# Optimization experiments

Hardware: AMD Instinct MI355X
Metric: run time of the kernel (lower is better)

The kernel has to match this reference:

```python
import jax, jax.numpy as jnp
import numpy as np
from jax import lax

# dims: T timesteps, CIN=6 DoG channels, HxW image; F conv filters, K kernel
T, CIN, H, W_IN = 15, 6, 512, 512
F, K, PAD = 64, 5, 2
THRESH = 15.0
K_WTA, RADIUS = 5, 2  # self.k1, self.r1


def setup_inputs() -> dict:
    key = jax.random.key(0)
    k1, k2 = jax.random.split(key)
    # cumulative binary spike wave: once a unit spikes it stays 1 (SpykeTorch convention)
    ev = (jax.random.uniform(k1, (T, CIN, H, W_IN)) < 0.02).astype(jnp.float32)
    x = jnp.clip(jnp.cumsum(ev, axis=0), 0.0, 1.0)
    w = 0.8 + 0.05 * jax.random.normal(k2, (F, CIN, K, K), dtype=jnp.float32)
    return {"x": x, "w": w}


def _pool_pad(x, pad):
    # sf.pooling(x, 2, 2): max-pool 2x2 stride 2; sf.pad: zero pad
    x = lax.reduce_window(x, -jnp.inf, lax.max, (1, 1, 2, 2), (1, 1, 2, 2), 'VALID')
    return jnp.pad(x, ((0, 0), (0, 0), (pad, pad), (pad, pad)))


def _fire(pot, thr):
    # sf.fire(pot, thr, True): zero sub-threshold potentials, spikes = sign
    tp = jnp.where(pot < thr, 0.0, pot)
    return jnp.sign(tp), tp


def _pointwise_inhibition(pot):
    # keep, per spatial site, only the feature with the earliest (then strongest) spike
    T_ = pot.shape[0]
    max_vals = jnp.max(pot, axis=1, keepdims=True)      # [T,1,H,W]
    max_idx = jnp.argmax(pot, axis=1, keepdims=True)    # [T,1,H,W]
    clamp = jnp.sign(max_vals)                          # 1 where any feature active
    earliest = jnp.clip(T_ - jnp.sum(clamp, axis=0, keepdims=True), 0, T_ - 1).astype(jnp.int32)  # [1,1,H,W]
    winners = jnp.take_along_axis(max_idx, earliest, axis=0)  # [1,1,H,W] winning feature
    has_spike = clamp[-1:]                              # [1,1,H,W] any spike by last step
    ch = jnp.arange(pot.shape[1]).reshape(1, -1, 1, 1)
    coef = jnp.where(ch == winners, has_spike, 0.0)     # scatter of winner coeff
    return pot * coef


def _get_k_winners(pot, spikes, k, radius):
    # NMS-like radius-based k-winners-take-all over [F,H,W]
    T_ = pot.shape[0]
    earliest = jnp.clip(T_ - jnp.sum(spikes, axis=0, keepdims=True), 0, T_ - 1).astype(jnp.int32)
    values = jnp.take_along_axis(pot, earliest, axis=0)  # potential at earliest spike
    trunc = spikes * values
    v = jnp.max(trunc) * T_  # large bias favoring earlier spikes
    total = jnp.sum(trunc + spikes * v, axis=0)          # [F,H,W]
    Fc, Hh, Ww = total.shape
    feat = jnp.arange(Fc).reshape(-1, 1, 1)
    row = jnp.arange(Hh).reshape(1, -1, 1)
    col = jnp.arange(Ww).reshape(1, 1, -1)
    winners = []
    for _ in range(k):  # small fixed k (5), fine to unroll
        idx = jnp.argmax(total)
        val = jnp.reshape(total, (-1,))[idx]
        f, r, c = jnp.unravel_index(idx, total.shape)
        active = val != 0
        win = jnp.where(active, jnp.stack([f, r, c]).astype(jnp.int32),
                        jnp.full((3,), -1, jnp.int32))
        winners.append(win)
        suppress = (feat == f) | ((jnp.abs(row - r) <= radius) & (jnp.abs(col - c) <= radius))
        total = jnp.where(active & suppress, 0.0, total)
    return jnp.stack(winners)  # [k,3] with -1 rows when fewer winners exist


def reference(x, w):
    inp = _pool_pad(x, PAD)  # [T,6,260,260]
    pot = lax.conv_general_dilated(inp, w, (1, 1), 'VALID',
                                   dimension_numbers=('NCHW', 'OIHW', 'NCHW'))  # [T,F,256,256]
    spk, pot = _fire(pot, THRESH)
    pot = _pointwise_inhibition(pot)
    spk = jnp.sign(pot)
    winners = _get_k_winners(pot, spk, K_WTA, RADIUS)
    return spk, winners
```

## Files before the change

kernel.cpp:

```cpp
#include <hip/hip_runtime.h>
#include <hip/hip_bf16.h>

#define T_ 15
#define CIN_ 6
#define F_ 64
#define HW_ 256
#define PW_ 260
#define THRESH_ 15.0f
#define TAU_NEVER 15


__global__ __launch_bounds__(256) void pool_tau(const float* __restrict__ x,
                                                unsigned char* __restrict__ tau,
                                                unsigned long long* __restrict__ slots,
                                                unsigned int* __restrict__ gmaxp) {
    int idx = blockIdx.x * 256 + threadIdx.x;
    if (idx < 5) slots[idx] = 0ULL;
    if (idx == 5) *gmaxp = 0u;
    if (idx >= CIN_ * PW_ * PW_) return;
    int xx = idx % PW_;
    int rest = idx / PW_;
    int yy = rest % PW_;
    int c = rest / PW_;
    unsigned char tv = TAU_NEVER;
    if (xx >= 2 && xx < 258 && yy >= 2 && yy < 258) {
        int i = yy - 2, j = xx - 2;
        const float* b0 = x + ((size_t)c * 512 + 2 * i) * 512 + 2 * j;
        const size_t tstride = (size_t)CIN_ * 512 * 512;
        {
            const float* b = b0 + 14 * tstride;
            float2 a = *(const float2*)b;
            float2 d = *(const float2*)(b + 512);
            if (a.x > 0.f || a.y > 0.f || d.x > 0.f || d.y > 0.f) {
                int lo = 0, hi = 14;
                while (lo < hi) {
                    int mid = (lo + hi) >> 1;
                    const float* bm = b0 + (size_t)mid * tstride;
                    float2 am = *(const float2*)bm;
                    float2 dm = *(const float2*)(bm + 512);
                    bool on = (am.x > 0.f || am.y > 0.f || dm.x > 0.f || dm.y > 0.f);
                    if (on) hi = mid; else lo = mid + 1;
                }
                tv = (unsigned char)lo;
            }
        }
    }
    tau[idx] = tv;
}

__global__ __launch_bounds__(256, 3) void phaseA(const unsigned char* __restrict__ tau,
                                                 const float* __restrict__ w,
                                                 int* __restrict__ rec_wch,
                                                 float* __restrict__ rec_val,
                                                 int* __restrict__ rec_e,
                                                 unsigned int* __restrict__ gmaxp) {
    __shared__ float wl2[150 * 64];
    __shared__ unsigned char tw[CIN_ * 144];
    __shared__ float wmax[4];

    const int tid = threadIdx.x;
    const int lane = tid & 63;
    const int g = tid >> 6;
    const int gx = (g & 1) * 4;
    const int gy = (g >> 1) * 4;
    const int px0 = blockIdx.x * 8;
    const int py0 = blockIdx.y * 8;

    for (int idx = tid; idx < 9600; idx += 256) {
        int k = idx >> 6, f = idx & 63;
        wl2[idx] = w[f * 150 + k];
    }
    for (int idx = tid; idx < CIN_ * 144; idx += 256) {
        int c = idx / 144;
        int rem = idx - c * 144;
        int r = rem / 12;
        int xx = rem - r * 12;
        tw[idx] = tau[(c * PW_ + (py0 + r)) * PW_ + (px0 + xx)];
    }
    __syncthreads();

    unsigned int done = 0;
    int myw = -1, mye = T_;
    float myv = 0.0f;
    float wavemax = 0.0f;

    for (int t = 0; t < T_; ++t) {
        float acc[16];
#pragma unroll
        for (int i = 0; i < 16; ++i) acc[i] = 0.0f;

        for (int c = 0; c < CIN_; ++c) {
            float win[8][8];
            const unsigned char* tb = &tw[c * 144 + gy * 12 + gx];
#pragma unroll
            for (int r = 0; r < 8; ++r) {
                unsigned int lo = *(const unsigned int*)(tb + r * 12);
                unsigned int hi = *(const unsigned int*)(tb + r * 12 + 4);
#pragma unroll
                for (int b = 0; b < 4; ++b) {
                    win[r][b]     = (((lo >> (8 * b)) & 0xFF) <= (unsigned)t) ? 1.0f : 0.0f;
                    win[r][4 + b] = (((hi >> (8 * b)) & 0xFF) <= (unsigned)t) ? 1.0f : 0.0f;
                }
            }
#pragma unroll
            for (int ki = 0; ki < 5; ++ki)
#pragma unroll
                for (int kj = 0; kj < 5; ++kj) {
                    float wv = wl2[((c * 25 + ki * 5 + kj) << 6) + lane];
#pragma unroll
                    for (int py = 0; py < 4; ++py)
#pragma unroll
                        for (int px = 0; px < 4; ++px)
                            acc[py * 4 + px] += win[py + ki][px + kj] * wv;
                }
        }

#pragma unroll
        for (int i = 0; i < 16; ++i) {
            if (done & (1u << i)) continue;
            float v = acc[i];
            v = (v < THRESH_) ? 0.0f : v;
            if (__any(v > 0.0f)) {
                unsigned long long key =
                    ((unsigned long long)__float_as_uint(v) << 6) | (unsigned)(63 - lane);
#pragma unroll
                for (int m = 1; m < 64; m <<= 1) {
                    unsigned long long o = __shfl_xor(key, m, 64);
                    if (o > key) key = o;
                }
                float mv = __uint_as_float((unsigned int)(key >> 6));
                int wf = 63 - (int)(key & 63ULL);
                done |= (1u << i);
                if (lane == i) { myw = wf; myv = mv; mye = t; }
                wavemax = fmaxf(wavemax, mv);
            }
        }
        if (done == 0xFFFFu) break;
    }

    if (lane < 16) {
        int py = lane >> 2, px = lane & 3;
        int p = (py0 + gy + py) * HW_ + (px0 + gx + px);
        rec_wch[p] = myw;
        rec_val[p] = myv;
        rec_e[p] = mye;
    }
    if (lane == 0) wmax[g] = wavemax;
    __syncthreads();
    if (tid == 0) {
        float m = fmaxf(fmaxf(wmax[0], wmax[1]), fmaxf(wmax[2], wmax[3]));
        if (m > 0.0f) atomicMax(gmaxp, __float_as_uint(m));
    }
}

__global__ __launch_bounds__(256) void render(const int* __restrict__ rec_wch,
                                              const int* __restrict__ rec_e,
                                              float* __restrict__ out) {
    const int tid = threadIdx.x;
    const int t = blockIdx.y;
    const int px = blockIdx.x * 1024 + tid * 4;

    int4 wch4 = *(const int4*)(rec_wch + px);
    int4 e4   = *(const int4*)(rec_e + px);
    int s0 = (wch4.x >= 0 && t >= e4.x) ? wch4.x : -1;
    int s1 = (wch4.y >= 0 && t >= e4.y) ? wch4.y : -1;
    int s2 = (wch4.z >= 0 && t >= e4.z) ? wch4.z : -1;
    int s3 = (wch4.w >= 0 && t >= e4.w) ? wch4.w : -1;

    float* base = out + (((size_t)t * F_) << 16) + px;
#pragma unroll
    for (int f = 0; f < F_; ++f) {
        float4 v;
        v.x = (f == s0) ? 1.0f : 0.0f;
        v.y = (f == s1) ? 1.0f : 0.0f;
        v.z = (f == s2) ? 1.0f : 0.0f;
        v.w = (f == s3) ? 1.0f : 0.0f;
        *(float4*)(base + ((size_t)f << 16)) = v;
    }
}

__global__ __launch_bounds__(256) void compute_total(const int* __restrict__ rec_wch,
                                                     const float* __restrict__ rec_val,
                                                     const int* __restrict__ rec_e,
                                                     const unsigned int* __restrict__ gmaxp,
                                                     float* __restrict__ total) {
    int i = blockIdx.x * 256 + threadIdx.x;
    int wch = rec_wch[i];
    float g = __uint_as_float(*gmaxp);
    float v15 = 15.0f * g;
    float tot = 0.0f;
    if (wch >= 0) {
        int e = rec_e[i];
        float base = rec_val[i] + v15;
        for (int t = e; t < T_; ++t) tot += base;
    }
    total[i] = tot;
}

__global__ __launch_bounds__(256) void max_round(const float* __restrict__ total,
                                                 const int* __restrict__ rec_wch,
                                                 unsigned long long* __restrict__ slots,
                                                 int round) {
    __shared__ unsigned long long sred[256];
    int i = blockIdx.x * 256 + threadIdx.x;
    float v = total[i];
    unsigned long long key = 0ULL;
    if (v > 0.0f) {
        int fch = rec_wch[i];
        int r = i >> 8, c = i & 255;
        bool sup = false;
        for (int j = 0; j < round; ++j) {
            unsigned long long s = slots[j];
            if (s == 0ULL) continue;
            int fl = 0x7fffffff - (int)(unsigned int)(s & 0xffffffffu);
            int fj = fl >> 16, rj = (fl >> 8) & 255, cj = fl & 255;
            int dr = r - rj; if (dr < 0) dr = -dr;
            int dc = c - cj; if (dc < 0) dc = -dc;
            if (fch == fj || (dr <= 2 && dc <= 2)) sup = true;
        }
        if (!sup) {
            int fl = (fch << 16) | i;
            unsigned int comp = 0x7fffffffu - (unsigned int)fl;
            key = ((unsigned long long)__float_as_uint(v) << 32) | comp;
        }
    }
    sred[threadIdx.x] = key;
    __syncthreads();
    for (int s = 128; s > 0; s >>= 1) {
        if (threadIdx.x < s) {
            if (sred[threadIdx.x + s] > sred[threadIdx.x]) sred[threadIdx.x] = sred[threadIdx.x + s];
        }
        __syncthreads();
    }
    if (threadIdx.x == 0 && sred[0] != 0ULL)
        atomicMax(&slots[round], sred[0]);
}

__global__ void writer(const unsigned long long* __restrict__ slots,
                       float* __restrict__ out) {
    int r = threadIdx.x;
    if (r < 5) {
        unsigned long long s = slots[r];
        float* wout = out + (size_t)T_ * F_ * HW_ * HW_ + r * 3;
        if (s != 0ULL) {
            int fl = 0x7fffffff - (int)(unsigned int)(s & 0xffffffffu);
            wout[0] = (float)(fl >> 16);
            wout[1] = (float)((fl >> 8) & 255);
            wout[2] = (float)(fl & 255);
        } else {
            wout[0] = -1.0f; wout[1] = -1.0f; wout[2] = -1.0f;
        }
    }
}

extern "C" void kernel_launch(void* const* d_in, const int* in_sizes, int n_in,
                              void* d_out, int out_size, void* d_ws, size_t ws_size,
                              hipStream_t stream) {
    const float* x = (const float*)d_in[0];
    const float* w = (const float*)d_in[1];
    float* out = (float*)d_out;

    char* wsc = (char*)d_ws;
    unsigned char* tau = (unsigned char*)wsc;
    size_t off = (size_t)CIN_ * PW_ * PW_;
    int* rec_wch = (int*)(wsc + off);        off += 65536 * sizeof(int);
    float* rec_val = (float*)(wsc + off);    off += 65536 * sizeof(float);
    int* rec_e = (int*)(wsc + off);          off += 65536 * sizeof(int);
    float* total = (float*)(wsc + off);      off += 65536 * sizeof(float);
    unsigned long long* slots = (unsigned long long*)(wsc + off);  off += 5 * sizeof(unsigned long long);
    unsigned int* gmaxp = (unsigned int*)(wsc + off);

    pool_tau<<<(CIN_ * PW_ * PW_ + 255) / 256, 256, 0, stream>>>(x, tau, slots, gmaxp);
    phaseA<<<dim3(32, 32), 256, 0, stream>>>(tau, w, rec_wch, rec_val, rec_e, gmaxp);
    render<<<dim3(64, 15), 256, 0, stream>>>(rec_wch, rec_e, out);
    compute_total<<<256, 256, 0, stream>>>(rec_wch, rec_val, rec_e, gmaxp, total);
    for (int r = 0; r < 5; ++r)
        max_round<<<256, 256, 0, stream>>>(total, rec_wch, slots, r);
    writer<<<1, 64, 0, stream>>>(slots, out);
}
```

Baseline: 471.3 us.

## Fuse k-winner selection into one single-block kernel and use nontemporal stores

Replaces the total computation, five per-round max-reduction launches and the writer kernel with one 1024-thread block that keeps totals in registers and runs all five suppression rounds with shared-memory reductions. This removes several launches and global round-trips for slots and totals. The render kernel switches its one-hot output writes to nontemporal stores to avoid polluting cache. The risk is that a single block on one compute unit serialises the selection work, and the 64-entry per-thread arrays may spill.

```diff
diff --git a/kernel.cpp b/kernel.cpp
--- a/kernel.cpp
+++ b/kernel.cpp
@@ -9,14 +9,14 @@
 #define THRESH_ 15.0f
 #define TAU_NEVER 15
 
+typedef float v4f __attribute__((ext_vector_type(4)));
+
 
 __global__ __launch_bounds__(256) void pool_tau(const float* __restrict__ x,
                                                 unsigned char* __restrict__ tau,
-                                                unsigned long long* __restrict__ slots,
                                                 unsigned int* __restrict__ gmaxp) {
     int idx = blockIdx.x * 256 + threadIdx.x;
-    if (idx < 5) slots[idx] = 0ULL;
-    if (idx == 5) *gmaxp = 0u;
+    if (idx == 0) *gmaxp = 0u;
     if (idx >= CIN_ * PW_ * PW_) return;
     int xx = idx % PW_;
     int rest = idx / PW_;
@@ -27,22 +27,20 @@
         int i = yy - 2, j = xx - 2;
         const float* b0 = x + ((size_t)c * 512 + 2 * i) * 512 + 2 * j;
         const size_t tstride = (size_t)CIN_ * 512 * 512;
-        {
-            const float* b = b0 + 14 * tstride;
-            float2 a = *(const float2*)b;
-            float2 d = *(const float2*)(b + 512);
-            if (a.x > 0.f || a.y > 0.f || d.x > 0.f || d.y > 0.f) {
-                int lo = 0, hi = 14;
-                while (lo < hi) {
-                    int mid = (lo + hi) >> 1;
-                    const float* bm = b0 + (size_t)mid * tstride;
-                    float2 am = *(const float2*)bm;
-                    float2 dm = *(const float2*)(bm + 512);
-                    bool on = (am.x > 0.f || am.y > 0.f || dm.x > 0.f || dm.y > 0.f);
-                    if (on) hi = mid; else lo = mid + 1;
-                }
-                tv = (unsigned char)lo;
-            }
+        const float* b = b0 + 14 * tstride;
+        float2 a = *(const float2*)b;
+        float2 d = *(const float2*)(b + 512);
+        if (a.x > 0.f || a.y > 0.f || d.x > 0.f || d.y > 0.f) {
+            int lo = 0, hi = 14;
+            while (lo < hi) {
+                int mid = (lo + hi) >> 1;
+                const float* bm = b0 + (size_t)mid * tstride;
+                float2 am = *(const float2*)bm;
+                float2 dm = *(const float2*)(bm + 512);
+                bool on = (am.x > 0.f || am.y > 0.f || dm.x > 0.f || dm.y > 0.f);
+                if (on) hi = mid; else lo = mid + 1;
+            }
+            tv = (unsigned char)lo;
         }
     }
     tau[idx] = tv;
@@ -170,86 +168,88 @@
     float* base = out + (((size_t)t * F_) << 16) + px;
 #pragma unroll
     for (int f = 0; f < F_; ++f) {
-        float4 v;
+        v4f v;
         v.x = (f == s0) ? 1.0f : 0.0f;
         v.y = (f == s1) ? 1.0f : 0.0f;
         v.z = (f == s2) ? 1.0f : 0.0f;
         v.w = (f == s3) ? 1.0f : 0.0f;
-        *(float4*)(base + ((size_t)f << 16)) = v;
-    }
-}
-
-__global__ __launch_bounds__(256) void compute_total(const int* __restrict__ rec_wch,
-                                                     const float* __restrict__ rec_val,
-                                                     const int* __restrict__ rec_e,
-                                                     const unsigned int* __restrict__ gmaxp,
-                                                     float* __restrict__ total) {
-    int i = blockIdx.x * 256 + threadIdx.x;
-    int wch = rec_wch[i];
+        __builtin_nontemporal_store(v, (v4f*)(base + ((size_t)f << 16)));
+    }
+}
+
+__global__ __launch_bounds__(1024) void select_winners(const int* __restrict__ rec_wch,
+                                                       const float* __restrict__ rec_val,
+                                                       const int* __restrict__ rec_e,
+                                                       const unsigned int* __restrict__ gmaxp,
+                                                       float* __restrict__ out) {
+    __shared__ unsigned long long sred[1024];
+    __shared__ int wfj[5], wrj[5], wcj[5], wact[5];
+
+    const int tid = threadIdx.x;
     float g = __uint_as_float(*gmaxp);
     float v15 = 15.0f * g;
-    float tot = 0.0f;
-    if (wch >= 0) {
-        int e = rec_e[i];
-        float base = rec_val[i] + v15;
-        for (int t = e; t < T_; ++t) tot += base;
-    }
-    total[i] = tot;
-}
-
-__global__ __launch_bounds__(256) void max_round(const float* __restrict__ total,
-                                                 const int* __restrict__ rec_wch,
-                                                 unsigned long long* __restrict__ slots,
-                                                 int round) {
-    __shared__ unsigned long long sred[256];
-    int i = blockIdx.x * 256 + threadIdx.x;
-    float v = total[i];
-    unsigned long long key = 0ULL;
-    if (v > 0.0f) {
-        int fch = rec_wch[i];
-        int r = i >> 8, c = i & 255;
-        bool sup = false;
-        for (int j = 0; j < round; ++j) {
-            unsigned long long s = slots[j];
-            if (s == 0ULL) continue;
-            int fl = 0x7fffffff - (int)(unsigned int)(s & 0xffffffffu);
-            int fj = fl >> 16, rj = (fl >> 8) & 255, cj = fl & 255;
-            int dr = r - rj; if (dr < 0) dr = -dr;
-            int dc = c - cj; if (dc < 0) dc = -dc;
-            if (fch == fj || (dr <= 2 && dc <= 2)) sup = true;
-        }
-        if (!sup) {
-            int fl = (fch << 16) | i;
-            unsigned int comp = 0x7fffffffu - (unsigned int)fl;
-            key = ((unsigned long long)__float_as_uint(v) << 32) | comp;
-        }
-    }
-    sred[threadIdx.x] = key;
-    __syncthreads();
-    for (int s = 128; s > 0; s >>= 1) {
-        if (threadIdx.x < s) {
-            if (sred[threadIdx.x + s] > sred[threadIdx.x]) sred[threadIdx.x] = sred[threadIdx.x + s];
-        }
+
+    float tot[64];
+    signed char fc[64];
+#pragma unroll 4
+    for (int k = 0; k < 64; ++k) {
+        int i = k * 1024 + tid;
+        int wch = rec_wch[i];
+        float tt = 0.0f;
+        if (wch >= 0) {
+            int e = rec_e[i];
+            float base = rec_val[i] + v15;
+            for (int t = e; t < T_; ++t) tt += base;
+        }
+        tot[k] = tt;
+        fc[k] = (signed char)wch;
+    }
+
+    for (int round = 0; round < 5; ++round) {
+        unsigned long long key = 0ULL;
+        for (int k = 0; k < 64; ++k) {
+            float v = tot[k];
+            if (v <= 0.0f) continue;
+            int i = k * 1024 + tid;
+            int fch = fc[k];
+            int r = i >> 8, c = i & 255;
+            bool sup = false;
+            for (int j = 0; j < round; ++j) {
+                if (!wact[j]) continue;
+                int dr = r - wrj[j]; if (dr < 0) dr = -dr;
+                int dc = c - wcj[j]; if (dc < 0) dc = -dc;
+                if (fch == wfj[j] || (dr <= 2 && dc <= 2)) sup = true;
+            }
+            if (!sup) {
+                int fl = (fch << 16) | i;
+                unsigned int comp = 0x7fffffffu - (unsigned int)fl;
+                unsigned long long kk =
+                    ((unsigned long long)__float_as_uint(v) << 32) | comp;
+                if (kk > key) key = kk;
+            }
+        }
+        sred[tid] = key;
         __syncthreads();
-    }
-    if (threadIdx.x == 0 && sred[0] != 0ULL)
-        atomicMax(&slots[round], sred[0]);
-}
-
-__global__ void writer(const unsigned long long* __restrict__ slots,
-                       float* __restrict__ out) {
-    int r = threadIdx.x;
-    if (r < 5) {
-        unsigned long long s = slots[r];
-        float* wout = out + (size_t)T_ * F_ * HW_ * HW_ + r * 3;
-        if (s != 0ULL) {
-            int fl = 0x7fffffff - (int)(unsigned int)(s & 0xffffffffu);
-            wout[0] = (float)(fl >> 16);
-            wout[1] = (float)((fl >> 8) & 255);
-            wout[2] = (float)(fl & 255);
-        } else {
-            wout[0] = -1.0f; wout[1] = -1.0f; wout[2] = -1.0f;
-        }
+        for (int s = 512; s > 0; s >>= 1) {
+            if (tid < s) {
+                if (sred[tid + s] > sred[tid]) sred[tid] = sred[tid + s];
+            }
+            __syncthreads();
+        }
+        if (tid == 0) {
+            unsigned long long sk = sred[0];
+            float* wout = out + (size_t)T_ * F_ * HW_ * HW_ + round * 3;
+            if (sk != 0ULL) {
+                int fl = 0x7fffffff - (int)(unsigned int)(sk & 0xffffffffu);
+                int f = fl >> 16, r = (fl >> 8) & 255, c = fl & 255;
+                wfj[round] = f; wrj[round] = r; wcj[round] = c; wact[round] = 1;
+                wout[0] = (float)f; wout[1] = (float)r; wout[2] = (float)c;
+            } else {
+                wact[round] = 0;
+                wout[0] = -1.0f; wout[1] = -1.0f; wout[2] = -1.0f;
+            }
+        }
+        __syncthreads();
     }
 }
 
@@ -266,15 +266,10 @@
     int* rec_wch = (int*)(wsc + off);        off += 65536 * sizeof(int);
     float* rec_val = (float*)(wsc + off);    off += 65536 * sizeof(float);
     int* rec_e = (int*)(wsc + off);          off += 65536 * sizeof(int);
-    float* total = (float*)(wsc + off);      off += 65536 * sizeof(float);
-    unsigned long long* slots = (unsigned long long*)(wsc + off);  off += 5 * sizeof(unsigned long long);
     unsigned int* gmaxp = (unsigned int*)(wsc + off);
 
-    pool_tau<<<(CIN_ * PW_ * PW_ + 255) / 256, 256, 0, stream>>>(x, tau, slots, gmaxp);
+    pool_tau<<<(CIN_ * PW_ * PW_ + 255) / 256, 256, 0, stream>>>(x, tau, gmaxp);
     phaseA<<<dim3(32, 32), 256, 0, stream>>>(tau, w, rec_wch, rec_val, rec_e, gmaxp);
     render<<<dim3(64, 15), 256, 0, stream>>>(rec_wch, rec_e, out);
-    compute_total<<<256, 256, 0, stream>>>(rec_wch, rec_val, rec_e, gmaxp, total);
-    for (int r = 0; r < 5; ++r)
-        max_round<<<256, 256, 0, stream>>>(total, rec_wch, slots, r);
-    writer<<<1, 64, 0, stream>>>(slots, out);
-}
+    select_winners<<<1, 1024, 0, stream>>>(rec_wch, rec_val, rec_e, gmaxp, out);
+}
```

Result: slower. 764.2 us (+62.2%).

## Precompute packed winner keys and use wavefront-shuffle reductions in k-WTA rounds

Applied to the files above, without the earlier changes.

Spike rendering now uses nontemporal vector stores for the large 15x64x256x256 output. The total-potential pass is replaced by a kernel that packs value and location into 64-bit keys, four pixels per thread. Each max round then reads only those keys and decodes earlier winners once per thread instead of per pixel. The shared-memory tree reduction is replaced with wavefront shuffles and one atomicMax per wavefront. The key buffer is larger than the old total buffer, but the small per-round kernels launch fewer blocks and do less synchronisation.

```diff
diff --git a/kernel.cpp b/kernel.cpp
--- a/kernel.cpp
+++ b/kernel.cpp
@@ -8,6 +8,8 @@
 #define PW_ 260
 #define THRESH_ 15.0f
 #define TAU_NEVER 15
+
+typedef float v4f __attribute__((ext_vector_type(4)));
 
 
 __global__ __launch_bounds__(256) void pool_tau(const float* __restrict__ x,
@@ -27,22 +29,20 @@
         int i = yy - 2, j = xx - 2;
         const float* b0 = x + ((size_t)c * 512 + 2 * i) * 512 + 2 * j;
         const size_t tstride = (size_t)CIN_ * 512 * 512;
-        {
-            const float* b = b0 + 14 * tstride;
-            float2 a = *(const float2*)b;
-            float2 d = *(const float2*)(b + 512);
-            if (a.x > 0.f || a.y > 0.f || d.x > 0.f || d.y > 0.f) {
-                int lo = 0, hi = 14;
-                while (lo < hi) {
-                    int mid = (lo + hi) >> 1;
-                    const float* bm = b0 + (size_t)mid * tstride;
-                    float2 am = *(const float2*)bm;
-                    float2 dm = *(const float2*)(bm + 512);
-                    bool on = (am.x > 0.f || am.y > 0.f || dm.x > 0.f || dm.y > 0.f);
-                    if (on) hi = mid; else lo = mid + 1;
-                }
-                tv = (unsigned char)lo;
-            }
+        const float* b = b0 + 14 * tstride;
+        float2 a = *(const float2*)b;
+        float2 d = *(const float2*)(b + 512);
+        if (a.x > 0.f || a.y > 0.f || d.x > 0.f || d.y > 0.f) {
+            int lo = 0, hi = 14;
+            while (lo < hi) {
+                int mid = (lo + hi) >> 1;
+                const float* bm = b0 + (size_t)mid * tstride;
+                float2 am = *(const float2*)bm;
+                float2 dm = *(const float2*)(bm + 512);
+                bool on = (am.x > 0.f || am.y > 0.f || dm.x > 0.f || dm.y > 0.f);
+                if (on) hi = mid; else lo = mid + 1;
+            }
+            tv = (unsigned char)lo;
         }
     }
     tau[idx] = tv;
@@ -170,70 +170,83 @@
     float* base = out + (((size_t)t * F_) << 16) + px;
 #pragma unroll
     for (int f = 0; f < F_; ++f) {
-        float4 v;
+        v4f v;
         v.x = (f == s0) ? 1.0f : 0.0f;
         v.y = (f == s1) ? 1.0f : 0.0f;
         v.z = (f == s2) ? 1.0f : 0.0f;
         v.w = (f == s3) ? 1.0f : 0.0f;
-        *(float4*)(base + ((size_t)f << 16)) = v;
-    }
-}
-
-__global__ __launch_bounds__(256) void compute_total(const int* __restrict__ rec_wch,
-                                                     const float* __restrict__ rec_val,
-                                                     const int* __restrict__ rec_e,
-                                                     const unsigned int* __restrict__ gmaxp,
-                                                     float* __restrict__ total) {
-    int i = blockIdx.x * 256 + threadIdx.x;
-    int wch = rec_wch[i];
+        __builtin_nontemporal_store(v, (v4f*)(base + ((size_t)f << 16)));
+    }
+}
+
+__global__ __launch_bounds__(256) void build_keys(const int* __restrict__ rec_wch,
+                                                  const float* __restrict__ rec_val,
+                                                  const int* __restrict__ rec_e,
+                                                  const unsigned int* __restrict__ gmaxp,
+                                                  unsigned long long* __restrict__ keys) {
+    int i0 = (blockIdx.x * 256 + threadIdx.x) * 4;
     float g = __uint_as_float(*gmaxp);
     float v15 = 15.0f * g;
-    float tot = 0.0f;
-    if (wch >= 0) {
-        int e = rec_e[i];
-        float base = rec_val[i] + v15;
-        for (int t = e; t < T_; ++t) tot += base;
-    }
-    total[i] = tot;
-}
-
-__global__ __launch_bounds__(256) void max_round(const float* __restrict__ total,
-                                                 const int* __restrict__ rec_wch,
+    int4 wch4 = *(const int4*)(rec_wch + i0);
+    float4 val4 = *(const float4*)(rec_val + i0);
+    int4 e4 = *(const int4*)(rec_e + i0);
+#pragma unroll
+    for (int q = 0; q < 4; ++q) {
+        int wch = (q == 0) ? wch4.x : (q == 1) ? wch4.y : (q == 2) ? wch4.z : wch4.w;
+        float val = (q == 0) ? val4.x : (q == 1) ? val4.y : (q == 2) ? val4.z : val4.w;
+        int e = (q == 0) ? e4.x : (q == 1) ? e4.y : (q == 2) ? e4.z : e4.w;
+        unsigned long long key = 0ULL;
+        if (wch >= 0) {
+            float base = val + v15;
+            float tot = 0.0f;
+            for (int t = e; t < T_; ++t) tot += base;
+            if (tot > 0.0f) {
+                int fl = (wch << 16) | (i0 + q);
+                key = ((unsigned long long)__float_as_uint(tot) << 32)
+                    | (0x7fffffffu - (unsigned int)fl);
+            }
+        }
+        keys[i0 + q] = key;
+    }
+}
+
+__global__ __launch_bounds__(256) void max_round(const unsigned long long* __restrict__ keys,
                                                  unsigned long long* __restrict__ slots,
                                                  int round) {
-    __shared__ unsigned long long sred[256];
-    int i = blockIdx.x * 256 + threadIdx.x;
-    float v = total[i];
-    unsigned long long key = 0ULL;
-    if (v > 0.0f) {
-        int fch = rec_wch[i];
-        int r = i >> 8, c = i & 255;
+    int i0 = (blockIdx.x * 256 + threadIdx.x) * 4;
+
+    int wf[4], wr[4], wc[4];
+    int nprev = 0;
+    for (int j = 0; j < round; ++j) {
+        unsigned long long s = slots[j];
+        if (s == 0ULL) continue;
+        int fl = 0x7fffffff - (int)(unsigned int)(s & 0xffffffffu);
+        wf[nprev] = fl >> 16; wr[nprev] = (fl >> 8) & 255; wc[nprev] = fl & 255;
+        ++nprev;
+    }
+
+    unsigned long long best = 0ULL;
+#pragma unroll
+    for (int q = 0; q < 4; ++q) {
+        unsigned long long k = keys[i0 + q];
+        if (k == 0ULL) continue;
+        int fl = 0x7fffffff - (int)(unsigned int)(k & 0xffffffffu);
+        int fch = fl >> 16, r = (fl >> 8) & 255, c = fl & 255;
         bool sup = false;
-        for (int j = 0; j < round; ++j) {
-            unsigned long long s = slots[j];
-            if (s == 0ULL) continue;
-            int fl = 0x7fffffff - (int)(unsigned int)(s & 0xffffffffu);
-            int fj = fl >> 16, rj = (fl >> 8) & 255, cj = fl & 255;
-            int dr = r - rj; if (dr < 0) dr = -dr;
-            int dc = c - cj; if (dc < 0) dc = -dc;
-            if (fch == fj || (dr <= 2 && dc <= 2)) sup = true;
-        }
-        if (!sup) {
-            int fl = (fch << 16) | i;
-            unsigned int comp = 0x7fffffffu - (unsigned int)fl;
-            key = ((unsigned long long)__float_as_uint(v) << 32) | comp;
-        }
-    }
-    sred[threadIdx.x] = key;
-    __syncthreads();
-    for (int s = 128; s > 0; s >>= 1) {
-        if (threadIdx.x < s) {
-            if (sred[threadIdx.x + s] > sred[threadIdx.x]) sred[threadIdx.x] = sred[threadIdx.x + s];
-        }
-        __syncthreads();
-    }
-    if (threadIdx.x == 0 && sred[0] != 0ULL)
-        atomicMax(&slots[round], sred[0]);
+        for (int j = 0; j < nprev; ++j) {
+            int dr = r - wr[j]; if (dr < 0) dr = -dr;
+            int dc = c - wc[j]; if (dc < 0) dc = -dc;
+            if (fch == wf[j] || (dr <= 2 && dc <= 2)) sup = true;
+        }
+        if (!sup && k > best) best = k;
+    }
+#pragma unroll
+    for (int m = 1; m < 64; m <<= 1) {
+        unsigned long long o = __shfl_xor(best, m, 64);
+        if (o > best) best = o;
+    }
+    if ((threadIdx.x & 63) == 0 && best != 0ULL)
+        atomicMax(&slots[round], best);
 }
 
 __global__ void writer(const unsigned long long* __restrict__ slots,
@@ -266,15 +279,15 @@
     int* rec_wch = (int*)(wsc + off);        off += 65536 * sizeof(int);
     float* rec_val = (float*)(wsc + off);    off += 65536 * sizeof(float);
     int* rec_e = (int*)(wsc + off);          off += 65536 * sizeof(int);
-    float* total = (float*)(wsc + off);      off += 65536 * sizeof(float);
-    unsigned long long* slots = (unsigned long long*)(wsc + off);  off += 5 * sizeof(unsigned long long);
+    unsigned long long* keys = (unsigned long long*)(wsc + off);  off += 65536 * sizeof(unsigned long long);
+    unsigned long long* slots = (unsigned long long*)(wsc + off); off += 8 * sizeof(unsigned long long);
     unsigned int* gmaxp = (unsigned int*)(wsc + off);
 
     pool_tau<<<(CIN_ * PW_ * PW_ + 255) / 256, 256, 0, stream>>>(x, tau, slots, gmaxp);
     phaseA<<<dim3(32, 32), 256, 0, stream>>>(tau, w, rec_wch, rec_val, rec_e, gmaxp);
     render<<<dim3(64, 15), 256, 0, stream>>>(rec_wch, rec_e, out);
-    compute_total<<<256, 256, 0, stream>>>(rec_wch, rec_val, rec_e, gmaxp, total);
+    build_keys<<<64, 256, 0, stream>>>(rec_wch, rec_val, rec_e, gmaxp, keys);
     for (int r = 0; r < 5; ++r)
-        max_round<<<256, 256, 0, stream>>>(total, rec_wch, slots, r);
+        max_round<<<64, 256, 0, stream>>>(keys, slots, r);
     writer<<<1, 64, 0, stream>>>(slots, out);
 }
```

Result: no change. 473.2 us (+0.4%).
